# Kernel tuning notes

Measured on AMD Instinct MI355X. Metric: run time of the kernel, lower is better.

## Reference

```python
import jax, jax.numpy as jnp
import numpy as np

N_HEADS = 4
D_K = 32

def setup_inputs() -> dict:
    key = jax.random.key(0)
    k1, k2, k3 = jax.random.split(key, 3)
    B, C, H, W = 4, 128, 64, 64
    x = jax.random.normal(k1, (B, C, H, W), dtype=jnp.float32)
    # projection: Linear(C, n_heads*d_k*3)
    Wp = jax.random.normal(k2, (N_HEADS * D_K * 3, C), dtype=jnp.float32) * (1.0 / np.sqrt(C))
    bp = jnp.zeros((N_HEADS * D_K * 3,), dtype=jnp.float32)
    # output: Linear(n_heads*d_k, C)
    Wo = jax.random.normal(k3, (C, N_HEADS * D_K), dtype=jnp.float32) * (1.0 / np.sqrt(N_HEADS * D_K))
    bo = jnp.zeros((C,), dtype=jnp.float32)
    return {"x": x, "Wp": Wp, "bp": bp, "Wo": Wo, "bo": bo}

def reference(x, Wp, bp, Wo, bo):
    B, C, H, W = x.shape
    scale = D_K ** (-0.5)
    # (B, C, H, W) -> (B, N, C);  NOTE: self.norm is defined but never applied in the original forward
    xs = x.reshape(B, C, H * W).transpose(0, 2, 1)
    qkv = (xs @ Wp.T + bp).reshape(B, H * W, N_HEADS, 3 * D_K)
    q, k, v = jnp.split(qkv, 3, axis=-1)  # each (B, N, h, d)
    attn = jnp.einsum('bihd,bjhd->bijh', q, k) * scale
    # faithful to original: softmax over dim=1 (the query/i axis)
    attn = jax.nn.softmax(attn, axis=1)
    res = jnp.einsum('bijh,bjhd->bihd', attn, v).reshape(B, H * W, N_HEADS * D_K)
    res = res @ Wo.T + bo + xs
    return res.transpose(0, 2, 1).reshape(B, C, H, W)
```

## Files before the change

kernel.cpp:

```cpp
#include <hip/hip_runtime.h>

typedef __bf16 bf16_t;
typedef __bf16 bf16x8 __attribute__((ext_vector_type(8)));
typedef float  f32x4  __attribute__((ext_vector_type(4)));

#define MFMA16(a, b, c) __builtin_amdgcn_mfma_f32_16x16x32_bf16((a), (b), (c), 0, 0, 0)

__device__ __forceinline__ float exp2_f(float x) { return __builtin_amdgcn_exp2f(x); }

union BPack { bf16_t h[2]; unsigned u; };

constexpr int Bn = 4, Cc = 128, Nn = 4096, NH = 4, DK = 32;
constexpr float QSCALE = 0.176776695f * 1.44269504f;

__global__ __launch_bounds__(256) void k_qkv(const float* __restrict__ x,
                                             const float* __restrict__ Wp,
                                             const float* __restrict__ bp,
                                             bf16_t* __restrict__ q_s,
                                             bf16_t* __restrict__ k_s,
                                             bf16_t* __restrict__ vt_s)
{
    __shared__ __attribute__((aligned(16))) char smem[40960];
    const int n0 = blockIdx.x * 64;
    const int b  = blockIdx.y;
    const int h  = blockIdx.z;
    const int t  = threadIdx.x;
    const int w = t >> 6, lane = t & 63, a = lane & 15, g = lane >> 4;

    const float* xb = x + (size_t)b * Cc * Nn;
    #pragma unroll
    for (int it = 0; it < 16; ++it) {
        int c = ((t >> 6) + it * 4) * 2;
        int n = t & 63;
        BPack p;
        p.h[0] = (bf16_t)xb[(size_t)c * Nn + n0 + n];
        p.h[1] = (bf16_t)xb[(size_t)(c + 1) * Nn + n0 + n];
        unsigned byte = n * 256 + ((unsigned)(c * 2) ^ ((n & 7) << 4));
        *(unsigned*)(smem + byte) = p.u;
    }
    const float* wpg = Wp + (size_t)h * 96 * Cc;
    #pragma unroll
    for (int it = 0; it < 24; ++it) {
        int idx = t + it * 256;
        int row = idx >> 6;
        int col = (idx & 63) * 2;
        BPack p;
        p.h[0] = (bf16_t)wpg[row * Cc + col];
        p.h[1] = (bf16_t)wpg[row * Cc + col + 1];
        unsigned byte = 16384 + row * 256 + ((unsigned)(col * 2) ^ ((row & 7) << 4));
        *(unsigned*)(smem + byte) = p.u;
    }
    __syncthreads();

    f32x4 acc[6] = {};
    #pragma unroll
    for (int kc = 0; kc < 4; ++kc) {
        int cb = (kc * 32 + g * 8) * 2;
        int rowA = w * 16 + a;
        bf16x8 af = *(const bf16x8*)(smem + rowA * 256 + (cb ^ ((rowA & 7) << 4)));
        #pragma unroll
        for (int pt = 0; pt < 6; ++pt) {
            int rowB = pt * 16 + a;
            bf16x8 bfr = *(const bf16x8*)(smem + 16384 + rowB * 256 + (cb ^ ((rowB & 7) << 4)));
            acc[pt] = MFMA16(af, bfr, acc[pt]);
        }
    }

    const int bh = b * NH + h;
    #pragma unroll
    for (int pt = 0; pt < 4; ++pt) {
        const int which = pt >> 1;
        const int d = (pt & 1) * 16 + a;
        const float bias = bp[h * 96 + which * 32 + d];
        bf16_t* dst = which ? k_s : q_s;
        const float sc = which ? 1.0f : QSCALE;
        #pragma unroll
        for (int r = 0; r < 4; ++r) {
            int n = n0 + w * 16 + g * 4 + r;
            dst[((size_t)bh * Nn + n) * DK + d] = (bf16_t)((acc[pt][r] + bias) * sc);
        }
    }
    __syncthreads();
    bf16_t* vt_l = (bf16_t*)smem;
    #pragma unroll
    for (int pt = 4; pt < 6; ++pt) {
        const int d = (pt & 1) * 16 + a;
        const float bias = bp[h * 96 + 64 + d];
        #pragma unroll
        for (int r = 0; r < 4; ++r) {
            int nl = w * 16 + g * 4 + r;
            vt_l[d * 72 + nl] = (bf16_t)(acc[pt][r] + bias);
        }
    }
    __syncthreads();
    #pragma unroll
    for (int it = 0; it < 8; ++it) {
        int idx = t + it * 256;
        int d = idx >> 6, n = idx & 63;
        int m = n & 31;
        int col = ((m & 15) << 1) | (m >> 4);
        int jj = (n & 32) | col;
        vt_s[((size_t)bh * DK + d) * Nn + n0 + jj] = vt_l[d * 72 + n];
    }
}

__global__ __launch_bounds__(256) void k_stats(const bf16_t* __restrict__ q_s,
                                               const bf16_t* __restrict__ k_s,
                                               float* __restrict__ S_part)
{
    const int bx = blockIdx.x;
    const int is = bx & 3;
    const int jc = (bx >> 2) & 31;
    const int bh = bx >> 7;
    const int t = threadIdx.x, w = t >> 6, lane = t & 63, a = lane & 15, g = lane >> 4;
    const bf16_t* Q = q_s + (size_t)bh * Nn * DK;
    const bf16_t* K = k_s + (size_t)bh * Nn * DK;
    const int jb = jc * 128 + w * 32;
    bf16x8 kf0 = *(const bf16x8*)(K + (jb + a) * DK + g * 8);
    bf16x8 kf1 = *(const bf16x8*)(K + (jb + 16 + a) * DK + g * 8);
    f32x4 l0 = {}, l1 = {};
    const int ilo = is * (Nn / 4);
    #pragma unroll 4
    for (int i0 = ilo; i0 < ilo + Nn / 4; i0 += 16) {
        bf16x8 qf = *(const bf16x8*)(Q + (i0 + a) * DK + g * 8);
        f32x4 z = {};
        f32x4 t0 = MFMA16(qf, kf0, z);
        f32x4 t1 = MFMA16(qf, kf1, z);
        #pragma unroll
        for (int r = 0; r < 4; ++r) {
            l0[r] += exp2_f(t0[r]);
            l1[r] += exp2_f(t1[r]);
        }
    }
    float s0 = l0[0] + l0[1] + l0[2] + l0[3];
    float s1 = l1[0] + l1[1] + l1[2] + l1[3];
    s0 += __shfl_xor(s0, 16);
    s0 += __shfl_xor(s0, 32);
    s1 += __shfl_xor(s1, 16);
    s1 += __shfl_xor(s1, 32);
    if (g == 0) {
        float* Sp = S_part + ((size_t)is * 16 + bh) * Nn;
        Sp[jb + a]      = s0;
        Sp[jb + 16 + a] = s1;
    }
}

__global__ __launch_bounds__(256) void k_vscale(const float* __restrict__ S_part,
                                                bf16_t* __restrict__ vt_s)
{
    __shared__ float sinv[512];
    const int Jb = blockIdx.x;
    const int bh = blockIdx.y;
    const int t = threadIdx.x;
    if (t < 128) {
        #pragma unroll
        for (int k2 = 0; k2 < 4; ++k2) {
            int Jl = t * 4 + k2;
            int m = Jl & 31;
            int pJ = (Jl & ~31) | (m >> 1) | ((m & 1) << 4);
            int J = Jb * 512 + pJ;
            float s = 0.f;
            #pragma unroll
            for (int is = 0; is < 4; ++is)
                s += S_part[((size_t)is * 16 + bh) * Nn + J];
            sinv[Jl] = 1.0f / s;
        }
    }
    __syncthreads();
    bf16_t* vrow = vt_s + (size_t)bh * DK * Nn;
    #pragma unroll
    for (int it = 0; it < 8; ++it) {
        int idx = t + it * 256;
        int d = idx >> 6, Jg = (idx & 63) * 8;
        bf16_t* p = vrow + (size_t)d * Nn + Jb * 512 + Jg;
        bf16x8 v = *(const bf16x8*)p;
        #pragma unroll
        for (int k2 = 0; k2 < 8; ++k2) v[k2] = (bf16_t)((float)v[k2] * sinv[Jg + k2]);
        *(bf16x8*)p = v;
    }
}

template<int JSPAN>
__global__ __launch_bounds__(256, 4) void k_attn(const bf16_t* __restrict__ q_s,
                                                 const bf16_t* __restrict__ k_s,
                                                 const bf16_t* __restrict__ vt_s,
                                                 float* __restrict__ opart)
{
    constexpr int NJS = Nn / JSPAN;
    const int bx = blockIdx.x;
    const int js = bx % NJS;
    const int ic = (bx / NJS) & 15;
    const int bh = bx / (NJS * 16);
    const int b = bh >> 2, h = bh & 3;
    const int t = threadIdx.x, w = t >> 6, lane = t & 63, a = lane & 15, g = lane >> 4;
    const int ib = ic * 256 + w * 64;
    const bf16_t* Q  = q_s  + (size_t)bh * Nn * DK;
    const bf16_t* K  = k_s  + (size_t)bh * Nn * DK;
    const bf16_t* Vt = vt_s + (size_t)bh * DK * Nn;
    bf16x8 qf[4];
    #pragma unroll
    for (int it = 0; it < 4; ++it)
        qf[it] = *(const bf16x8*)(Q + (size_t)(ib + it * 16 + a) * DK + g * 8);
    f32x4 o0[4] = {}, o1[4] = {};
    auto compute = [&](bf16x8 ck0, bf16x8 ck1, bf16x8 cv0, bf16x8 cv1) {
        f32x4 z = {};
        #pragma unroll
        for (int it = 0; it < 4; ++it) {
            f32x4 s0 = MFMA16(ck0, qf[it], z);
            f32x4 s1 = MFMA16(ck1, qf[it], z);
            bf16x8 pa;
            #pragma unroll
            for (int r = 0; r < 4; ++r) {
                pa[2 * r]     = (bf16_t)exp2_f(s0[r]);
                pa[2 * r + 1] = (bf16_t)exp2_f(s1[r]);
            }
            o0[it] = MFMA16(pa, cv0, o0[it]);
            o1[it] = MFMA16(pa, cv1, o1[it]);
        }
    };
    const int jlo = js * JSPAN;
    bf16x8 kf0 = *(const bf16x8*)(K + (size_t)(jlo + a) * DK + g * 8);
    bf16x8 kf1 = *(const bf16x8*)(K + (size_t)(jlo + 16 + a) * DK + g * 8);
    bf16x8 vf0 = *(const bf16x8*)(Vt + (size_t)a * Nn + jlo + g * 8);
    bf16x8 vf1 = *(const bf16x8*)(Vt + (size_t)(16 + a) * Nn + jlo + g * 8);
    #pragma unroll 2
    for (int j0 = jlo; j0 < jlo + JSPAN - 32; j0 += 32) {
        bf16x8 ck0 = kf0, ck1 = kf1, cv0 = vf0, cv1 = vf1;
        kf0 = *(const bf16x8*)(K + (size_t)(j0 + 32 + a) * DK + g * 8);
        kf1 = *(const bf16x8*)(K + (size_t)(j0 + 48 + a) * DK + g * 8);
        vf0 = *(const bf16x8*)(Vt + (size_t)a * Nn + j0 + 32 + g * 8);
        vf1 = *(const bf16x8*)(Vt + (size_t)(16 + a) * Nn + j0 + 32 + g * 8);
        compute(ck0, ck1, cv0, cv1);
    }
    compute(kf0, kf1, vf0, vf1);

    float* Ob = opart + ((size_t)(js * Bn + b) * Nn) * 128 + h * DK;
    #pragma unroll
    for (int it = 0; it < 4; ++it) {
        #pragma unroll
        for (int r = 0; r < 4; ++r) {
            int n = ib + it * 16 + g * 4 + r;
            Ob[(size_t)n * 128 + a]      = o0[it][r];
            Ob[(size_t)n * 128 + 16 + a] = o1[it][r];
        }
    }
}

__global__ __launch_bounds__(256) void k_out(const float* __restrict__ opart,
                                             const float* __restrict__ Wo,
                                             const float* __restrict__ bo,
                                             const float* __restrict__ x,
                                             float* __restrict__ out,
                                             int NJS)
{
    __shared__ __attribute__((aligned(16))) char smem[33280];
    const int n0 = blockIdx.x * 64;
    const int b = blockIdx.y;
    const int t = threadIdx.x, w = t >> 6, lane = t & 63, a = lane & 15, g = lane >> 4;
    #pragma unroll
    for (int it = 0; it < 32; ++it) {
        int idx = t + it * 256;
        int row = idx >> 6;
        int col = (idx & 63) * 2;
        BPack p;
        p.h[0] = (bf16_t)Wo[row * 128 + col];
        p.h[1] = (bf16_t)Wo[row * 128 + col + 1];
        unsigned byte = row * 256 + ((unsigned)(col * 2) ^ ((row & 7) << 4));
        *(unsigned*)(smem + byte) = p.u;
    }
    __syncthreads();
    const size_t OSTRIDE = (size_t)Bn * Nn * 128;
    const float* Ob = opart + ((size_t)b * Nn + n0 + w * 16 + a) * 128;
    f32x4 acc[8] = {};
    #pragma unroll
    for (int kc = 0; kc < 4; ++kc) {
        f32x4 sA = {}, sB = {};
        for (int js = 0; js < NJS; ++js) {
            const float* pp = Ob + (size_t)js * OSTRIDE + kc * 32 + g * 8;
            sA += *(const f32x4*)pp;
            sB += *(const f32x4*)(pp + 4);
        }
        bf16x8 af;
        #pragma unroll
        for (int k2 = 0; k2 < 4; ++k2) {
            af[k2]     = (bf16_t)sA[k2];
            af[k2 + 4] = (bf16_t)sB[k2];
        }
        int cb = (kc * 32 + g * 8) * 2;
        #pragma unroll
        for (int ct = 0; ct < 8; ++ct) {
            int rowB = ct * 16 + a;
            bf16x8 bfr = *(const bf16x8*)(smem + rowB * 256 + (cb ^ ((rowB & 7) << 4)));
            acc[ct] = MFMA16(af, bfr, acc[ct]);
        }
    }
    __syncthreads();
    float* out_t = (float*)smem;
    #pragma unroll
    for (int ct = 0; ct < 8; ++ct) {
        int c = ct * 16 + a;
        #pragma unroll
        for (int r = 0; r < 4; ++r) {
            out_t[c * 65 + w * 16 + g * 4 + r] = acc[ct][r];
        }
    }
    __syncthreads();
    const float* xb = x + (size_t)b * Cc * Nn;
    #pragma unroll
    for (int it = 0; it < 32; ++it) {
        int idx = t + it * 256;
        int c = idx >> 6, n = idx & 63;
        out[((size_t)b * Cc + c) * Nn + n0 + n] = out_t[c * 65 + n] + xb[(size_t)c * Nn + n0 + n] + bo[c];
    }
}

extern "C" void kernel_launch(void* const* d_in, const int* in_sizes, int n_in,
                              void* d_out, int out_size, void* d_ws, size_t ws_size,
                              hipStream_t stream)
{
    const float* x  = (const float*)d_in[0];
    const float* Wp = (const float*)d_in[1];
    const float* bp = (const float*)d_in[2];
    const float* Wo = (const float*)d_in[3];
    const float* bo = (const float*)d_in[4];
    float* out = (float*)d_out;

    char* ws = (char*)d_ws;
    bf16_t* q_s   = (bf16_t*)(ws);
    bf16_t* k_s   = (bf16_t*)(ws + (4  << 20));
    bf16_t* vt_s  = (bf16_t*)(ws + (8  << 20));
    float*  S_part= (float*) (ws + (12 << 20));
    float*  opart = (float*) (ws + (13 << 20));

    const size_t base = 13ull << 20;
    const size_t plane = 8ull << 20;
    int NJS = 1;
    if (ws_size >= base + 4 * plane) NJS = 4;
    else if (ws_size >= base + 2 * plane) NJS = 2;

    k_qkv   <<<dim3(Nn / 64, Bn, NH),   256, 0, stream>>>(x, Wp, bp, q_s, k_s, vt_s);
    k_stats <<<16 * 32 * 4,             256, 0, stream>>>(q_s, k_s, S_part);
    k_vscale<<<dim3(8, 16),             256, 0, stream>>>(S_part, vt_s);
    if (NJS == 4)      k_attn<1024><<<16 * 16 * 4, 256, 0, stream>>>(q_s, k_s, vt_s, opart);
    else if (NJS == 2) k_attn<2048><<<16 * 16 * 2, 256, 0, stream>>>(q_s, k_s, vt_s, opart);
    else               k_attn<4096><<<16 * 16 * 1, 256, 0, stream>>>(q_s, k_s, vt_s, opart);
    k_out   <<<dim3(Nn / 64, Bn),       256, 0, stream>>>(opart, Wo, bo, x, out, NJS);
}
```

Measured before the change: 189.9 us.

## Store attention partials as packed bf16 and allow eight key splits

The attention kernel now writes its per-split partial outputs as bf16 pairs packed into 32-bit words instead of fp32, halving the partial buffer size. The output kernel unpacks the halves with bit shifts before summing. Because each plane is smaller, the launcher can pick eight key-span splits (JSPAN 512) when the workspace allows, which raises grid parallelism in the attention kernel. The cost is bf16 rounding of the partial sums before the reduction, and more partial planes to read in the output kernel.

```diff
diff --git a/kernel.cpp b/kernel.cpp
--- a/kernel.cpp
+++ b/kernel.cpp
@@ -3,6 +3,7 @@
 typedef __bf16 bf16_t;
 typedef __bf16 bf16x8 __attribute__((ext_vector_type(8)));
 typedef float  f32x4  __attribute__((ext_vector_type(4)));
+typedef unsigned u32x4 __attribute__((ext_vector_type(4)));
 
 #define MFMA16(a, b, c) __builtin_amdgcn_mfma_f32_16x16x32_bf16((a), (b), (c), 0, 0, 0)
 
@@ -184,7 +185,7 @@
 __global__ __launch_bounds__(256, 4) void k_attn(const bf16_t* __restrict__ q_s,
                                                  const bf16_t* __restrict__ k_s,
                                                  const bf16_t* __restrict__ vt_s,
-                                                 float* __restrict__ opart)
+                                                 unsigned* __restrict__ opart)
 {
     constexpr int NJS = Nn / JSPAN;
     const int bx = blockIdx.x;
@@ -234,19 +235,21 @@
     }
     compute(kf0, kf1, vf0, vf1);
 
-    float* Ob = opart + ((size_t)(js * Bn + b) * Nn) * 128 + h * DK;
+    unsigned* Ob = opart + ((size_t)(js * Bn + b) * Nn) * 64 + h * 16 + a;
     #pragma unroll
     for (int it = 0; it < 4; ++it) {
         #pragma unroll
         for (int r = 0; r < 4; ++r) {
             int n = ib + it * 16 + g * 4 + r;
-            Ob[(size_t)n * 128 + a]      = o0[it][r];
-            Ob[(size_t)n * 128 + 16 + a] = o1[it][r];
-        }
-    }
-}
-
-__global__ __launch_bounds__(256) void k_out(const float* __restrict__ opart,
+            BPack p;
+            p.h[0] = (bf16_t)o0[it][r];
+            p.h[1] = (bf16_t)o1[it][r];
+            Ob[(size_t)n * 64] = p.u;
+        }
+    }
+}
+
+__global__ __launch_bounds__(256) void k_out(const unsigned* __restrict__ opart,
                                              const float* __restrict__ Wo,
                                              const float* __restrict__ bo,
                                              const float* __restrict__ x,
@@ -269,23 +272,27 @@
         *(unsigned*)(smem + byte) = p.u;
     }
     __syncthreads();
-    const size_t OSTRIDE = (size_t)Bn * Nn * 128;
-    const float* Ob = opart + ((size_t)b * Nn + n0 + w * 16 + a) * 128;
+    const size_t OSTR32 = (size_t)Bn * Nn * 64;
+    const unsigned* Ob = opart + ((size_t)b * Nn + n0 + w * 16 + a) * 64;
+    const unsigned hi = (g >= 2);
+    const int wsub = (g & 1) * 8;
     f32x4 acc[8] = {};
     #pragma unroll
     for (int kc = 0; kc < 4; ++kc) {
-        f32x4 sA = {}, sB = {};
+        float s[8] = {};
         for (int js = 0; js < NJS; ++js) {
-            const float* pp = Ob + (size_t)js * OSTRIDE + kc * 32 + g * 8;
-            sA += *(const f32x4*)pp;
-            sB += *(const f32x4*)(pp + 4);
+            const unsigned* pp = Ob + (size_t)js * OSTR32 + kc * 16 + wsub;
+            u32x4 v0 = *(const u32x4*)pp;
+            u32x4 v1 = *(const u32x4*)(pp + 4);
+            #pragma unroll
+            for (int k2 = 0; k2 < 4; ++k2) {
+                s[k2]     += __uint_as_float(hi ? (v0[k2] & 0xffff0000u) : (v0[k2] << 16));
+                s[k2 + 4] += __uint_as_float(hi ? (v1[k2] & 0xffff0000u) : (v1[k2] << 16));
+            }
         }
         bf16x8 af;
         #pragma unroll
-        for (int k2 = 0; k2 < 4; ++k2) {
-            af[k2]     = (bf16_t)sA[k2];
-            af[k2 + 4] = (bf16_t)sB[k2];
-        }
+        for (int k2 = 0; k2 < 8; ++k2) af[k2] = (bf16_t)s[k2];
         int cb = (kc * 32 + g * 8) * 2;
         #pragma unroll
         for (int ct = 0; ct < 8; ++ct) {
@@ -326,22 +333,24 @@
     float* out = (float*)d_out;
 
     char* ws = (char*)d_ws;
-    bf16_t* q_s   = (bf16_t*)(ws);
-    bf16_t* k_s   = (bf16_t*)(ws + (4  << 20));
-    bf16_t* vt_s  = (bf16_t*)(ws + (8  << 20));
-    float*  S_part= (float*) (ws + (12 << 20));
-    float*  opart = (float*) (ws + (13 << 20));
+    bf16_t*  q_s   = (bf16_t*)(ws);
+    bf16_t*  k_s   = (bf16_t*)(ws + (4  << 20));
+    bf16_t*  vt_s  = (bf16_t*)(ws + (8  << 20));
+    float*   S_part= (float*) (ws + (12 << 20));
+    unsigned* opart= (unsigned*)(ws + (13 << 20));
 
     const size_t base = 13ull << 20;
-    const size_t plane = 8ull << 20;
+    const size_t plane = 4ull << 20;
     int NJS = 1;
-    if (ws_size >= base + 4 * plane) NJS = 4;
+    if (ws_size >= base + 8 * plane) NJS = 8;
+    else if (ws_size >= base + 4 * plane) NJS = 4;
     else if (ws_size >= base + 2 * plane) NJS = 2;
 
     k_qkv   <<<dim3(Nn / 64, Bn, NH),   256, 0, stream>>>(x, Wp, bp, q_s, k_s, vt_s);
     k_stats <<<16 * 32 * 4,             256, 0, stream>>>(q_s, k_s, S_part);
     k_vscale<<<dim3(8, 16),             256, 0, stream>>>(S_part, vt_s);
-    if (NJS == 4)      k_attn<1024><<<16 * 16 * 4, 256, 0, stream>>>(q_s, k_s, vt_s, opart);
+    if (NJS == 8)      k_attn<512> <<<16 * 16 * 8, 256, 0, stream>>>(q_s, k_s, vt_s, opart);
+    else if (NJS == 4) k_attn<1024><<<16 * 16 * 4, 256, 0, stream>>>(q_s, k_s, vt_s, opart);
     else if (NJS == 2) k_attn<2048><<<16 * 16 * 2, 256, 0, stream>>>(q_s, k_s, vt_s, opart);
     else               k_attn<4096><<<16 * 16 * 1, 256, 0, stream>>>(q_s, k_s, vt_s, opart);
     k_out   <<<dim3(Nn / 64, Bn),       256, 0, stream>>>(opart, Wo, bo, x, out, NJS);
```

After: 196.2 us. +3.3%, slower.
